# Optimization experiments

Measured on AMD Instinct MI355X. Metric: run time of the kernel, lower is better.

## Reference

```python
import jax, jax.numpy as jnp
import numpy as np

B, T, A, K, STEPS, E = 2, 16384, 128, 128, 16, 126


def soft_dirac_last(x):
    # softmax forward-replaced by one-hot(argmax), straight-through backward
    sm = jax.nn.softmax(x, axis=-1)
    hard = jax.nn.one_hot(jnp.argmax(x, axis=-1), x.shape[-1], dtype=x.dtype)
    return sm + jax.lax.stop_gradient(hard - sm)


def _encode(x, d_unit, atom_embeddings):
    # x: (B,1,T); d_unit: (A,K) unit-norm atoms
    rng = jnp.linspace(0.0, 1.0, T, dtype=x.dtype)
    kernel = d_unit[:, None, :]  # OIH
    pad = [(K // 2, K - 1 - K // 2)]  # SAME
    batch_ix = jnp.arange(B)

    def step(res, _):
        # dense feature map: correlation of residual with every atom
        fm = jax.lax.conv_general_dilated(
            res, kernel, window_strides=(1,), padding=pad,
            dimension_numbers=("NCH", "OIH", "NCH"))  # (B,A,T)
        flat = fm.reshape(B, A * T)
        fi = jnp.argmax(flat, axis=-1)                      # sparsify n_to_keep=1
        value = jnp.take_along_axis(flat, fi[:, None], axis=-1)  # (B,1)
        ai = fi // T
        ti = fi % T
        # position: soft_dirac over time of sparse fm summed over atoms
        pos_row = jnp.zeros((B, T), x.dtype).at[batch_ix, ti].set(value[:, 0])
        pd = soft_dirac_last(pos_row)
        position = jnp.sum(pd * rng[None, :], axis=-1, keepdims=True) * 20.0  # (B,1)
        # atom one-hot: soft_dirac over atom axis of sparse fm summed over time
        atom_row = jnp.zeros((B, A), x.dtype).at[batch_ix, ai].set(value[:, 0])
        ad = soft_dirac_last(atom_row)
        ae = ad @ atom_embeddings  # (B,E)
        emb = jnp.concatenate([position, value, ae], axis=-1)  # (B, 2+E)
        # matching-pursuit residual update: subtract value * atom at found shift
        recon = value * d_unit[ai]  # (B,K)
        buf = jnp.zeros((B, T + K), x.dtype)
        buf = jax.vmap(lambda bb, rr, tt: jax.lax.dynamic_update_slice(bb, rr, (tt,)))(buf, recon, ti)
        res = res - buf[:, None, K // 2:K // 2 + T]
        return res, emb

    res, embs = jax.lax.scan(step, x, None, length=STEPS)
    embs = jnp.transpose(embs, (1, 0, 2))  # (B, STEPS, 2+E)
    return embs, res


def _canonical_ordering(embs, proj):
    keys = embs @ proj  # (B, STEPS)
    order = jnp.argsort(keys, axis=-1)
    return jnp.take_along_axis(embs, order[:, :, None], axis=1)


def setup_inputs() -> dict:
    key = jax.random.key(0)
    ks = jax.random.split(key, 5)
    return {
        "a": jax.random.normal(ks[0], (B, 1, T), jnp.float32),
        "b": jax.random.normal(ks[1], (B, 1, T), jnp.float32),
        "d": jax.random.normal(ks[2], (A, K), jnp.float32),
        "atom_embeddings": jax.random.normal(ks[3], (A, E), jnp.float32) * 0.1,
        "ordering_proj": jax.random.normal(ks[4], (128,), jnp.float32),
    }


def reference(a, b, d, atom_embeddings, ordering_proj):
    d_unit = d / (jnp.linalg.norm(d, axis=-1, keepdims=True) + 1e-8)
    ae, a_res = _encode(a, d_unit, atom_embeddings)
    be, b_res = _encode(b, d_unit, atom_embeddings)
    ae = _canonical_ordering(ae, ordering_proj)
    be = _canonical_ordering(be, ordering_proj)
    a_norm = jnp.linalg.norm(a_res.reshape(-1, T), axis=-1)
    b_norm = jnp.linalg.norm(b_res.reshape(-1, T), axis=-1)
    return jnp.mean((ae - be) ** 2) + jnp.mean(jnp.abs(a_norm - b_norm))
```

## Files before the change

kernel.cpp:

```cpp
#include <hip/hip_runtime.h>
#include <math.h>

#define T_DIM 16384
#define A_DIM 128
#define K_DIM 128
#define N_STEPS 16
#define E_DIM 126
#define NSEQ 4

#define NPT0 512
#define NAT8 16
#define TT 256
#define NTT 64
#define HB 8192
#define RL_LEN 8319
#define SS_LEN 383
#define SPAD 16

#define PIDX(i) ((i) + ((i) >> 5))

#define NB_STEP0 (NPT0 * NSEQ)
#define NB_INC   (65 * NSEQ)
#define NB_TOTAL (NB_STEP0 + NB_INC + 1)

#define SM_U64 4448

__device__ inline unsigned long long pack_vi(float v, int fi) {
    unsigned int b = __float_as_uint(v);
    b = (b & 0x80000000u) ? ~b : (b | 0x80000000u);
    return ((unsigned long long)b << 32) | (unsigned int)(~fi);
}
__device__ inline void unpack_vi(unsigned long long p, float* v, int* fi) {
    unsigned int lo = (unsigned int)(p & 0xffffffffu);
    unsigned int b = (unsigned int)(p >> 32);
    unsigned int fb = (b & 0x80000000u) ? (b & 0x7fffffffu) : ~b;
    *v = __uint_as_float(fb);
    *fi = (int)(~lo);
}
__device__ inline unsigned long long u64max(unsigned long long a, unsigned long long b) {
    return a > b ? a : b;
}
__device__ inline unsigned long long pollu64(const unsigned long long* p) {
    unsigned long long v = __hip_atomic_load(p, __ATOMIC_RELAXED,
                                             __HIP_MEMORY_SCOPE_AGENT);
    while (v == 0ULL) {
        __builtin_amdgcn_s_sleep(1);
        v = __hip_atomic_load(p, __ATOMIC_RELAXED, __HIP_MEMORY_SCOPE_AGENT);
    }
    return v;
}

__global__ __launch_bounds__(256) void k_prep(
    const float* __restrict__ d, float* __restrict__ du,
    unsigned long long* __restrict__ arena) {
    int blk = blockIdx.x, tid = threadIdx.x;
    if (blk < 128) {
        __shared__ float s[128];
        float v = 0.0f;
        if (tid < 128) { v = d[blk * K_DIM + tid]; s[tid] = v * v; }
        __syncthreads();
        for (int off = 64; off > 0; off >>= 1) {
            if (tid < off) s[tid] += s[tid + off];
            __syncthreads();
        }
        if (tid < 128) du[blk * K_DIM + tid] = v / (sqrtf(s[0]) + 1e-8f);
    } else {
        int zb = blk - 128;
        for (int i = zb * 256 + tid; i < 31744; i += 64 * 256)
            arena[2048 + i] = 0ULL;
        if (blk == 128) {
            int* ctrl = (int*)(arena + 33792);
            if (tid < NSEQ) {
                ctrl[tid * 32] = 0;
                ((float*)ctrl)[160 + tid * 32] = 0.0f;
            }
            if (tid == 4) ctrl[128] = 0;
        }
    }
}

__device__ inline unsigned long long tile16(
    const float* __restrict__ duP, const float* __restrict__ rsh,
    int L0, int a_lo, int t_lo, int tid, unsigned long long* red4) {
    float acc[4][4];
    #pragma unroll
    for (int i = 0; i < 4; i++)
        #pragma unroll
        for (int j = 0; j < 4; j++) acc[i][j] = 0.0f;
    float r[8];
    #pragma unroll
    for (int m = 0; m < 8; m++) r[m] = rsh[PIDX(L0 + m)];
    #pragma unroll 4
    for (int k = 0; k < K_DIM; k += 4) {
        float dA[4][4];
        #pragma unroll
        for (int i = 0; i < 4; i++)
            *(float4*)dA[i] = *(const float4*)(duP + i * K_DIM + k);
        #pragma unroll
        for (int dk = 0; dk < 4; dk++) {
            #pragma unroll
            for (int i = 0; i < 4; i++) {
                float s = dA[i][dk];
                #pragma unroll
                for (int j = 0; j < 4; j++)
                    acc[i][j] = fmaf(s, r[j + dk], acc[i][j]);
            }
        }
        r[0] = r[4]; r[1] = r[5]; r[2] = r[6]; r[3] = r[7];
        #pragma unroll
        for (int m = 0; m < 4; m++) r[4 + m] = rsh[PIDX(L0 + k + 8 + m)];
    }
    float bv = -INFINITY;
    int bi = 0x7fffffff;
    #pragma unroll
    for (int i = 0; i < 4; i++) {
        int aa = a_lo + i;
        #pragma unroll
        for (int j = 0; j < 4; j++) {
            int fi = aa * T_DIM + t_lo + j;
            float v = acc[i][j];
            if (v > bv || (v == bv && fi < bi)) { bv = v; bi = fi; }
        }
    }
    #pragma unroll
    for (int off = 32; off > 0; off >>= 1) {
        float v2 = __shfl_down(bv, off);
        int   i2 = __shfl_down(bi, off);
        if (v2 > bv || (v2 == bv && i2 < bi)) { bv = v2; bi = i2; }
    }
    if ((tid & 63) == 0) red4[tid >> 6] = pack_vi(bv, bi);
    __syncthreads();
    if (tid == 0) {
        unsigned long long m = red4[0];
        #pragma unroll
        for (int w = 1; w < 4; w++) m = u64max(m, red4[w]);
        red4[0] = m;
    }
    __syncthreads();
    return red4[0];
}

__device__ inline unsigned long long tile8(
    const float* __restrict__ duP, const float* __restrict__ rsh,
    int L0, int a_lo, int t_lo, int tid, unsigned long long* red4) {
    float acc[2][4];
    #pragma unroll
    for (int i = 0; i < 2; i++)
        #pragma unroll
        for (int j = 0; j < 4; j++) acc[i][j] = 0.0f;
    float r[8];
    #pragma unroll
    for (int m = 0; m < 8; m++) r[m] = rsh[PIDX(L0 + m)];
    #pragma unroll 4
    for (int k = 0; k < K_DIM; k += 4) {
        float dA[2][4];
        #pragma unroll
        for (int i = 0; i < 2; i++)
            *(float4*)dA[i] = *(const float4*)(duP + i * K_DIM + k);
        #pragma unroll
        for (int dk = 0; dk < 4; dk++) {
            #pragma unroll
            for (int i = 0; i < 2; i++) {
                float s = dA[i][dk];
                #pragma unroll
                for (int j = 0; j < 4; j++)
                    acc[i][j] = fmaf(s, r[j + dk], acc[i][j]);
            }
        }
        r[0] = r[4]; r[1] = r[5]; r[2] = r[6]; r[3] = r[7];
        #pragma unroll
        for (int m = 0; m < 4; m++) r[4 + m] = rsh[PIDX(L0 + k + 8 + m)];
    }
    float bv = -INFINITY;
    int bi = 0x7fffffff;
    #pragma unroll
    for (int i = 0; i < 2; i++) {
        int aa = a_lo + i;
        #pragma unroll
        for (int j = 0; j < 4; j++) {
            int fi = aa * T_DIM + t_lo + j;
            float v = acc[i][j];
            if (v > bv || (v == bv && fi < bi)) { bv = v; bi = fi; }
        }
    }
    #pragma unroll
    for (int off = 32; off > 0; off >>= 1) {
        float v2 = __shfl_down(bv, off);
        int   i2 = __shfl_down(bi, off);
        if (v2 > bv || (v2 == bv && i2 < bi)) { bv = v2; bi = i2; }
    }
    if ((tid & 63) == 0) red4[tid >> 6] = pack_vi(bv, bi);
    __syncthreads();
    if (tid == 0) {
        unsigned long long m = red4[0];
        #pragma unroll
        for (int w = 1; w < 4; w++) m = u64max(m, red4[w]);
        red4[0] = m;
    }
    __syncthreads();
    return red4[0];
}

__global__ __launch_bounds__(256) void k_mega(
    const float* __restrict__ a, const float* __restrict__ b,
    const float* __restrict__ du, const float* __restrict__ ae,
    const float* __restrict__ proj, float* __restrict__ emb,
    unsigned long long* __restrict__ arena, float* __restrict__ out) {

    __shared__ unsigned long long SMEM[SM_U64];
    unsigned long long* pmax = arena;
    unsigned long long* dsl  = arena + 2048;
    unsigned long long* wsl  = arena + 32768;
    unsigned long long* w0   = arena + 33728;
    int*   cnt   = (int*)(arena + 33792);
    int*   done  = cnt + 128;
    float* norm2 = (float*)cnt + 160;

    int blk = blockIdx.x;
    int tid = threadIdx.x;

    if (blk < NB_STEP0) {
        int seq = blk >> 9;
        int idx = blk & 511;
        int a_base = (idx >> 6) * 16;
        int t0 = (idx & 63) * TT;
        float* rsh = (float*)SMEM;
        unsigned long long* pm_sh = SMEM + 256;
        unsigned long long* red4  = SMEM + 512;
        int* flag = (int*)(SMEM + 516);

        const float* x = (seq < 2 ? a : b) + (seq & 1) * T_DIM;
        for (int i = tid; i < SS_LEN; i += 256) {
            int t = t0 - 64 + i;
            rsh[PIDX(i)] = (t >= 0 && t < T_DIM) ? x[t] : 0.0f;
        }
        __syncthreads();
        int tg = tid & 63;
        int ag = __builtin_amdgcn_readfirstlane(tid >> 6);
        unsigned long long p = tile16(du + (a_base + ag * 4) * K_DIM, rsh,
                                      4 * tg, a_base + ag * 4, t0 + 4 * tg,
                                      tid, red4);
        if (tid == 0) {
            pmax[seq * NPT0 + idx] = p;
            __threadfence();
            flag[0] = (atomicAdd(&cnt[seq * 32], 1) == NPT0 - 1);
        }
        __syncthreads();
        if (!flag[0]) return;

        __threadfence();
        pm_sh[tid] = u64max(pmax[seq * NPT0 + tid], pmax[seq * NPT0 + 256 + tid]);
        __syncthreads();
        for (int off = 128; off > 0; off >>= 1) {
            if (tid < off) pm_sh[tid] = u64max(pm_sh[tid], pm_sh[tid + off]);
            __syncthreads();
        }
        float value; int fi;
        unpack_vi(pm_sh[0], &value, &fi);
        int ai = fi >> 14, ti = fi & (T_DIM - 1);
        int pos_idx = value > 0.0f ? ti : 0;
        int atom_idx = value > 0.0f ? ai : 0;
        float* e = emb + (seq * N_STEPS + 0) * 128;
        if (tid == 0) {
            e[0] = ((float)pos_idx / (float)(T_DIM - 1)) * 20.0f;
            e[1] = value;
        }
        if (tid >= 2 && tid < 2 + E_DIM) e[tid] = ae[atom_idx * E_DIM + tid - 2];
        __syncthreads();
        __threadfence();
        if (tid == 0) atomicExch(&w0[seq * SPAD], pm_sh[0]);
        return;
    }

    if (blk < NB_STEP0 + NB_INC) {
        int r = blk - NB_STEP0;
        int seq = r / 65;
        int sub = r - seq * 65;

        if (sub == 64) {
            unsigned long long* table   = SMEM;
            unsigned long long* poll_sh = SMEM + 512;
            unsigned long long* red4    = SMEM + 548;
            unsigned long long* wbc     = SMEM + 552;

            if (tid == 0) wbc[0] = pollu64(&w0[seq * SPAD]);
            __syncthreads();
            __threadfence();
            for (int i = tid; i < NPT0; i += 256) table[i] = pmax[seq * NPT0 + i];
            float v0; int fi0;
            unpack_vi(wbc[0], &v0, &fi0);
            int ti = fi0 & (T_DIM - 1);
            int lo = ti - 127; if (lo < 0) lo = 0;
            int hi = ti + 128; if (hi > T_DIM) hi = T_DIM;
            __syncthreads();

            for (int step = 1; step < N_STEPS; step++) {
                int T0 = lo >> 8, T1 = T0 + 1;
                bool hasT1 = (T1 < NTT) && (T1 * TT < hi);
                if (tid < 32) {
                    if (((tid & 1) == 0) || hasT1)
                        poll_sh[tid] = pollu64(
                            &dsl[(((step - 1) * NSEQ + seq) * 32 + tid) * SPAD]);
                }
                __syncthreads();
                if (tid < 16) {
                    int at16 = tid >> 1, ts = tid & 1;
                    if (ts == 0 || hasT1)
                        table[at16 * 64 + (ts ? T1 : T0)] =
                            u64max(poll_sh[at16 * 4 + ts], poll_sh[at16 * 4 + 2 + ts]);
                }
                __syncthreads();
                unsigned long long m = u64max(table[tid], table[tid + 256]);
                #pragma unroll
                for (int off = 32; off > 0; off >>= 1)
                    m = u64max(m, __shfl_down(m, off));
                if ((tid & 63) == 0) red4[tid >> 6] = m;
                __syncthreads();
                if (tid == 0) {
                    unsigned long long w = red4[0];
                    #pragma unroll
                    for (int j = 1; j < 4; j++) w = u64max(w, red4[j]);
                    red4[0] = w;
                    atomicExch(&wsl[((step - 1) * NSEQ + seq) * SPAD], w);
                }
                __syncthreads();
                float value; int fi;
                unpack_vi(red4[0], &value, &fi);
                int wt = fi & (T_DIM - 1);
                int wa = fi >> 14;
                int pos_idx = value > 0.0f ? wt : 0;
                int atom_idx = value > 0.0f ? wa : 0;
                float* e = emb + (seq * N_STEPS + step) * 128;
                if (tid == 0) {
                    e[0] = ((float)pos_idx / (float)(T_DIM - 1)) * 20.0f;
                    e[1] = value;
                }
                if (tid >= 2 && tid < 128) e[tid] = ae[atom_idx * E_DIM + tid - 2];
                lo = wt - 127; if (lo < 0) lo = 0;
                hi = wt + 128; if (hi > T_DIM) hi = T_DIM;
            }
            __syncthreads();
            __threadfence();
            if (tid == 0) atomicAdd(done, 1);
            return;
        }

        int atile = sub >> 2;
        int half = (sub >> 1) & 1;
        int par = sub & 1;
        int a_base = atile * 8;
        int base = half * HB;
        float* resL = (float*)SMEM;
        unsigned long long* red4 = SMEM + 4304;
        unsigned long long* wshp = SMEM + 4308;
        float* snorm = (float*)(SMEM + 4320);

        const float* x = (seq < 2 ? a : b) + (seq & 1) * T_DIM;
        for (int i = tid; i < RL_LEN; i += 256) {
            int t = base - 64 + i;
            resL[PIDX(i)] = (t >= 0 && t < T_DIM) ? x[t] : 0.0f;
        }
        if (tid == 0) wshp[0] = pollu64(&w0[seq * SPAD]);
        __syncthreads();
        float v0; int fi0;
        unpack_vi(wshp[0], &v0, &fi0);
        int ti0 = fi0 & (T_DIM - 1), ai0 = fi0 >> 14;
        if (tid < 128) {
            int t = ti0 - 64 + tid;
            if (t >= 0 && t < T_DIM) {
                int L = t - base + 64;
                if (L >= 0 && L < RL_LEN) {
                    float rr = resL[PIDX(L)];
                    resL[PIDX(L)] = __fsub_rn(rr, __fmul_rn(v0, du[ai0 * K_DIM + tid]));
                }
            }
        }
        __syncthreads();
        int lo = ti0 - 127; if (lo < 0) lo = 0;
        int hi = ti0 + 128; if (hi > T_DIM) hi = T_DIM;

        for (int step = 1; step < N_STEPS; step++) {
            int T0 = lo >> 8, T1 = T0 + 1;
            int cand = -1;
            if (((T0 & 1) == par) && ((T0 >> 5) == half)) cand = T0;
            else if (T1 < NTT && ((T1 & 1) == par) && ((T1 >> 5) == half) &&
                     T1 * TT < hi) cand = T1;

            if (cand >= 0) {
                int t0 = cand * TT;
                int tg = tid & 63;
                int ag = __builtin_amdgcn_readfirstlane(tid >> 6);
                unsigned long long p = tile8(
                    du + (a_base + ag * 2) * K_DIM, resL,
                    (t0 - base) + 4 * tg, a_base + ag * 2, t0 + 4 * tg, tid, red4);
                if (tid == 0)
                    atomicExch(&dsl[(((step - 1) * NSEQ + seq) * 32 +
                                     atile * 2 + (cand == T1 ? 1 : 0)) * SPAD], p);
            }
            if (tid == 0) wshp[0] = pollu64(&wsl[((step - 1) * NSEQ + seq) * SPAD]);
            __syncthreads();
            float value; int fi;
            unpack_vi(wshp[0], &value, &fi);
            int wt = fi & (T_DIM - 1);
            int wa = fi >> 14;
            if (tid < 128) {
                int t = wt - 64 + tid;
                if (t >= 0 && t < T_DIM) {
                    int L = t - base + 64;
                    if (L >= 0 && L < RL_LEN) {
                        float rr = resL[PIDX(L)];
                        resL[PIDX(L)] = __fsub_rn(rr, __fmul_rn(value, du[wa * K_DIM + tid]));
                    }
                }
            }
            __syncthreads();
            lo = wt - 127; if (lo < 0) lo = 0;
            hi = wt + 128; if (hi > T_DIM) hi = T_DIM;
        }

        if (atile == 0 && par == 0) {
            float s = 0.0f;
            for (int t = tid; t < HB; t += 256) {
                float v = resL[PIDX(t + 64)];
                s = fmaf(v, v, s);
            }
            snorm[tid] = s;
            __syncthreads();
            for (int off = 128; off > 0; off >>= 1) {
                if (tid < off) snorm[tid] += snorm[tid + off];
                __syncthreads();
            }
            if (tid == 0) {
                float old = atomicAdd(&norm2[seq * 32], snorm[0]);
                if (__float_as_uint(old) != 0xFFFFFFFFu)
                    atomicAdd(done, 1);
            }
        }
        return;
    }

    {
        float* keys  = (float*)SMEM;
        int*   order = (int*)(SMEM + 32);
        float* sh    = (float*)(SMEM + 64);
        float* norms = (float*)(SMEM + 192);

        if (tid == 0) {
            int c = __hip_atomic_load(done, __ATOMIC_RELAXED, __HIP_MEMORY_SCOPE_AGENT);
            while (c < 12) {
                __builtin_amdgcn_s_sleep(8);
                c = __hip_atomic_load(done, __ATOMIC_RELAXED, __HIP_MEMORY_SCOPE_AGENT);
            }
        }
        __syncthreads();
        __threadfence();

        if (tid < NSEQ)
            norms[tid] = sqrtf(__hip_atomic_load(&norm2[tid * 32], __ATOMIC_RELAXED,
                                                 __HIP_MEMORY_SCOPE_AGENT));
        if (tid < 64) {
            int seq = tid >> 4, st = tid & 15;
            const float* e = emb + (seq * N_STEPS + st) * 128;
            float kk = 0.0f;
            for (int dd = 0; dd < 128; dd++) kk = fmaf(e[dd], proj[dd], kk);
            keys[tid] = kk;
        }
        __syncthreads();
        if (tid < NSEQ) {
            int ord[N_STEPS];
            for (int i = 0; i < N_STEPS; i++) ord[i] = i;
            for (int i = 1; i < N_STEPS; i++) {
                int oi = ord[i];
                float kv = keys[tid * N_STEPS + oi];
                int j = i - 1;
                while (j >= 0 && keys[tid * N_STEPS + ord[j]] > kv) {
                    ord[j + 1] = ord[j]; j--;
                }
                ord[j + 1] = oi;
            }
            for (int i = 0; i < N_STEPS; i++) order[tid * N_STEPS + i] = ord[i];
        }
        __syncthreads();
        float s = 0.0f;
        #pragma unroll
        for (int t = 0; t < 16; t++) {
            int idx = tid + t * 256;
            int bq = idx >> 11;
            int st = (idx >> 7) & 15;
            int dd = idx & 127;
            float va = emb[((bq    ) * N_STEPS + order[bq * N_STEPS + st]) * 128 + dd];
            float vb = emb[((2 + bq) * N_STEPS + order[(2 + bq) * N_STEPS + st]) * 128 + dd];
            float df = va - vb;
            s = fmaf(df, df, s);
        }
        sh[tid] = s;
        __syncthreads();
        for (int off = 128; off > 0; off >>= 1) {
            if (tid < off) sh[tid] += sh[tid + off];
            __syncthreads();
        }
        if (tid == 0) {
            float mse = sh[0] / 4096.0f;
            float mad = 0.5f * (fabsf(norms[0] - norms[2]) + fabsf(norms[1] - norms[3]));
            out[0] = mse + mad;
        }
    }
}

extern "C" void kernel_launch(void* const* d_in, const int* in_sizes, int n_in,
                              void* d_out, int out_size, void* d_ws, size_t ws_size,
                              hipStream_t stream) {
    const float* a    = (const float*)d_in[0];
    const float* b    = (const float*)d_in[1];
    const float* d    = (const float*)d_in[2];
    const float* ae   = (const float*)d_in[3];
    const float* proj = (const float*)d_in[4];
    float* out = (float*)d_out;

    float* ws  = (float*)d_ws;
    float* du  = ws;
    float* emb = du + A_DIM * K_DIM;
    unsigned long long* arena = (unsigned long long*)(emb + NSEQ * N_STEPS * 128);

    k_prep<<<192, 256, 0, stream>>>(d, du, arena);
    k_mega<<<NB_TOTAL, 256, 0, stream>>>(a, b, du, ae, proj, emb, arena, out);
}
```

Measured before the change: 216.7 us.

## Replicate argmax reduction in every worker block to drop coordinator broadcast hop

Each worker block now waits on the step-0 completion counter, reads the full partial-max table itself, and at each later step polls all per-tile partial maxima and reduces them locally. The separate coordinator-to-worker winner broadcast (wsl/w0) is no longer on the critical path. This removes one global-memory round trip of cross-block latency per matching-pursuit step. In exchange every block does redundant polling and reduction and keeps a 512-entry table in shared memory, which raises shared memory use and global polling traffic.

```diff
diff --git a/kernel.cpp b/kernel.cpp
--- a/kernel.cpp
+++ b/kernel.cpp
@@ -23,7 +23,7 @@
 #define NB_INC   (65 * NSEQ)
 #define NB_TOTAL (NB_STEP0 + NB_INC + 1)
 
-#define SM_U64 4448
+#define SM_U64 4960
 
 __device__ inline unsigned long long pack_vi(float v, int fi) {
     unsigned int b = __float_as_uint(v);
@@ -48,6 +48,13 @@
         v = __hip_atomic_load(p, __ATOMIC_RELAXED, __HIP_MEMORY_SCOPE_AGENT);
     }
     return v;
+}
+__device__ inline void pollcnt(const int* p, int target) {
+    int v = __hip_atomic_load(p, __ATOMIC_RELAXED, __HIP_MEMORY_SCOPE_AGENT);
+    while (v < target) {
+        __builtin_amdgcn_s_sleep(1);
+        v = __hip_atomic_load(p, __ATOMIC_RELAXED, __HIP_MEMORY_SCOPE_AGENT);
+    }
 }
 
 __global__ __launch_bounds__(256) void k_prep(
@@ -210,7 +217,6 @@
     __shared__ unsigned long long SMEM[SM_U64];
     unsigned long long* pmax = arena;
     unsigned long long* dsl  = arena + 2048;
-    unsigned long long* wsl  = arena + 32768;
     unsigned long long* w0   = arena + 33728;
     int*   cnt   = (int*)(arena + 33792);
     int*   done  = cnt + 128;
@@ -281,18 +287,32 @@
             unsigned long long* table   = SMEM;
             unsigned long long* poll_sh = SMEM + 512;
             unsigned long long* red4    = SMEM + 548;
-            unsigned long long* wbc     = SMEM + 552;
-
-            if (tid == 0) wbc[0] = pollu64(&w0[seq * SPAD]);
+
+            if (tid == 0) pollcnt(&cnt[seq * 32], NPT0);
             __syncthreads();
             __threadfence();
             for (int i = tid; i < NPT0; i += 256) table[i] = pmax[seq * NPT0 + i];
+            __syncthreads();
+            {
+                unsigned long long m0 = u64max(table[tid], table[tid + 256]);
+                #pragma unroll
+                for (int off = 32; off > 0; off >>= 1)
+                    m0 = u64max(m0, __shfl_down(m0, off));
+                if ((tid & 63) == 0) red4[tid >> 6] = m0;
+            }
+            __syncthreads();
+            if (tid == 0) {
+                unsigned long long w = red4[0];
+                #pragma unroll
+                for (int j = 1; j < 4; j++) w = u64max(w, red4[j]);
+                red4[0] = w;
+            }
+            __syncthreads();
             float v0; int fi0;
-            unpack_vi(wbc[0], &v0, &fi0);
+            unpack_vi(red4[0], &v0, &fi0);
             int ti = fi0 & (T_DIM - 1);
             int lo = ti - 127; if (lo < 0) lo = 0;
             int hi = ti + 128; if (hi > T_DIM) hi = T_DIM;
-            __syncthreads();
 
             for (int step = 1; step < N_STEPS; step++) {
                 int T0 = lo >> 8, T1 = T0 + 1;
@@ -321,7 +341,6 @@
                     #pragma unroll
                     for (int j = 1; j < 4; j++) w = u64max(w, red4[j]);
                     red4[0] = w;
-                    atomicExch(&wsl[((step - 1) * NSEQ + seq) * SPAD], w);
                 }
                 __syncthreads();
                 float value; int fi;
@@ -351,8 +370,9 @@
         int a_base = atile * 8;
         int base = half * HB;
         float* resL = (float*)SMEM;
-        unsigned long long* red4 = SMEM + 4304;
-        unsigned long long* wshp = SMEM + 4308;
+        unsigned long long* red4   = SMEM + 4304;
+        unsigned long long* pollsh = SMEM + 4320;
+        unsigned long long* table  = SMEM + 4448;
         float* snorm = (float*)(SMEM + 4320);
 
         const float* x = (seq < 2 ? a : b) + (seq & 1) * T_DIM;
@@ -360,10 +380,28 @@
             int t = base - 64 + i;
             resL[PIDX(i)] = (t >= 0 && t < T_DIM) ? x[t] : 0.0f;
         }
-        if (tid == 0) wshp[0] = pollu64(&w0[seq * SPAD]);
+        if (tid == 0) pollcnt(&cnt[seq * 32], NPT0);
+        __syncthreads();
+        __threadfence();
+        for (int i = tid; i < NPT0; i += 256) table[i] = pmax[seq * NPT0 + i];
+        __syncthreads();
+        {
+            unsigned long long m0 = u64max(table[tid], table[tid + 256]);
+            #pragma unroll
+            for (int off = 32; off > 0; off >>= 1)
+                m0 = u64max(m0, __shfl_down(m0, off));
+            if ((tid & 63) == 0) red4[tid >> 6] = m0;
+        }
+        __syncthreads();
+        if (tid == 0) {
+            unsigned long long w = red4[0];
+            #pragma unroll
+            for (int j = 1; j < 4; j++) w = u64max(w, red4[j]);
+            red4[0] = w;
+        }
         __syncthreads();
         float v0; int fi0;
-        unpack_vi(wshp[0], &v0, &fi0);
+        unpack_vi(red4[0], &v0, &fi0);
         int ti0 = fi0 & (T_DIM - 1), ai0 = fi0 >> 14;
         if (tid < 128) {
             int t = ti0 - 64 + tid;
@@ -381,6 +419,7 @@
 
         for (int step = 1; step < N_STEPS; step++) {
             int T0 = lo >> 8, T1 = T0 + 1;
+            bool hasT1 = (T1 < NTT) && (T1 * TT < hi);
             int cand = -1;
             if (((T0 & 1) == par) && ((T0 >> 5) == half)) cand = T0;
             else if (T1 < NTT && ((T1 & 1) == par) && ((T1 >> 5) == half) &&
@@ -397,10 +436,34 @@
                     atomicExch(&dsl[(((step - 1) * NSEQ + seq) * 32 +
                                      atile * 2 + (cand == T1 ? 1 : 0)) * SPAD], p);
             }
-            if (tid == 0) wshp[0] = pollu64(&wsl[((step - 1) * NSEQ + seq) * SPAD]);
+            if (tid < 32) {
+                if (((tid & 1) == 0) || hasT1)
+                    pollsh[tid] = pollu64(
+                        &dsl[(((step - 1) * NSEQ + seq) * 32 + tid) * SPAD]);
+            }
+            __syncthreads();
+            if (tid < 16) {
+                int at16 = tid >> 1, ts = tid & 1;
+                if (ts == 0 || hasT1)
+                    table[at16 * 64 + (ts ? T1 : T0)] =
+                        u64max(pollsh[at16 * 4 + ts], pollsh[at16 * 4 + 2 + ts]);
+            }
+            __syncthreads();
+            unsigned long long m = u64max(table[tid], table[tid + 256]);
+            #pragma unroll
+            for (int off = 32; off > 0; off >>= 1)
+                m = u64max(m, __shfl_down(m, off));
+            if ((tid & 63) == 0) red4[tid >> 6] = m;
+            __syncthreads();
+            if (tid == 0) {
+                unsigned long long w = red4[0];
+                #pragma unroll
+                for (int j = 1; j < 4; j++) w = u64max(w, red4[j]);
+                red4[0] = w;
+            }
             __syncthreads();
             float value; int fi;
-            unpack_vi(wshp[0], &value, &fi);
+            unpack_vi(red4[0], &value, &fi);
             int wt = fi & (T_DIM - 1);
             int wa = fi >> 14;
             if (tid < 128) {
```

Measured after the change: 226.4 us. 4.5% more time.

## Double block size to 512 threads, stage atoms in LDS, prefetch atom loads

Applied to the files above, without the earlier changes.

Moves k_mega from 256 to 512 threads per block and halves each wave's atom count, so eight waves share a tile. The unit-norm atom rows are copied into shared memory and read from there with a one-step register prefetch, instead of coming straight from global memory. All reductions and shared-memory offsets are resized for eight waves, and the spin-wait now polls a few times before it starts sleeping. The aim is more latency hiding and less global traffic in the correlation tiles, at the cost of higher shared-memory use per block and more barrier participants.

```diff
diff --git a/kernel.cpp b/kernel.cpp
--- a/kernel.cpp
+++ b/kernel.cpp
@@ -9,13 +9,13 @@
 #define NSEQ 4
 
 #define NPT0 512
-#define NAT8 16
 #define TT 256
 #define NTT 64
 #define HB 8192
 #define RL_LEN 8319
 #define SS_LEN 383
 #define SPAD 16
+#define NTHR 512
 
 #define PIDX(i) ((i) + ((i) >> 5))
 
@@ -23,7 +23,7 @@
 #define NB_INC   (65 * NSEQ)
 #define NB_TOTAL (NB_STEP0 + NB_INC + 1)
 
-#define SM_U64 4448
+#define SM_U64 4960
 
 __device__ inline unsigned long long pack_vi(float v, int fi) {
     unsigned int b = __float_as_uint(v);
@@ -43,8 +43,9 @@
 __device__ inline unsigned long long pollu64(const unsigned long long* p) {
     unsigned long long v = __hip_atomic_load(p, __ATOMIC_RELAXED,
                                              __HIP_MEMORY_SCOPE_AGENT);
+    int spins = 0;
     while (v == 0ULL) {
-        __builtin_amdgcn_s_sleep(1);
+        if (++spins > 4) __builtin_amdgcn_s_sleep(1);
         v = __hip_atomic_load(p, __ATOMIC_RELAXED, __HIP_MEMORY_SCOPE_AGENT);
     }
     return v;
@@ -79,42 +80,55 @@
     }
 }
 
-__device__ inline unsigned long long tile16(
-    const float* __restrict__ duP, const float* __restrict__ rsh,
-    int L0, int a_lo, int t_lo, int tid, unsigned long long* red4) {
-    float acc[4][4];
+template<int APW>
+__device__ inline unsigned long long tileW(
+    const float* __restrict__ duL,
+    const float* __restrict__ rsh,
+    int L0, int a_blk, int t_lo, int tid, unsigned long long* red8) {
+    int ag = __builtin_amdgcn_readfirstlane(tid >> 6);
+    const float* dp = duL + (ag * APW) * K_DIM;
+    float acc[APW][4];
     #pragma unroll
-    for (int i = 0; i < 4; i++)
+    for (int i = 0; i < APW; i++)
         #pragma unroll
         for (int j = 0; j < 4; j++) acc[i][j] = 0.0f;
-    float r[8];
+    float r[12];
     #pragma unroll
-    for (int m = 0; m < 8; m++) r[m] = rsh[PIDX(L0 + m)];
+    for (int m = 0; m < 12; m++) r[m] = rsh[PIDX(L0 + m)];
+    float4 dnx[APW];
+    #pragma unroll
+    for (int i = 0; i < APW; i++)
+        dnx[i] = *(const float4*)(dp + i * K_DIM);
     #pragma unroll 4
     for (int k = 0; k < K_DIM; k += 4) {
-        float dA[4][4];
-        #pragma unroll
-        for (int i = 0; i < 4; i++)
-            *(float4*)dA[i] = *(const float4*)(duP + i * K_DIM + k);
+        float dc[APW][4];
+        #pragma unroll
+        for (int i = 0; i < APW; i++) *(float4*)dc[i] = dnx[i];
+        if (k + 4 < K_DIM) {
+            #pragma unroll
+            for (int i = 0; i < APW; i++)
+                dnx[i] = *(const float4*)(dp + i * K_DIM + k + 4);
+        }
         #pragma unroll
         for (int dk = 0; dk < 4; dk++) {
             #pragma unroll
-            for (int i = 0; i < 4; i++) {
-                float s = dA[i][dk];
+            for (int i = 0; i < APW; i++) {
+                float s = dc[i][dk];
                 #pragma unroll
                 for (int j = 0; j < 4; j++)
                     acc[i][j] = fmaf(s, r[j + dk], acc[i][j]);
             }
         }
-        r[0] = r[4]; r[1] = r[5]; r[2] = r[6]; r[3] = r[7];
-        #pragma unroll
-        for (int m = 0; m < 4; m++) r[4 + m] = rsh[PIDX(L0 + k + 8 + m)];
+        #pragma unroll
+        for (int m = 0; m < 8; m++) r[m] = r[4 + m];
+        #pragma unroll
+        for (int m = 0; m < 4; m++) r[8 + m] = rsh[PIDX(L0 + k + 12 + m)];
     }
     float bv = -INFINITY;
     int bi = 0x7fffffff;
     #pragma unroll
-    for (int i = 0; i < 4; i++) {
-        int aa = a_lo + i;
+    for (int i = 0; i < APW; i++) {
+        int aa = a_blk + ag * APW + i;
         #pragma unroll
         for (int j = 0; j < 4; j++) {
             int fi = aa * T_DIM + t_lo + j;
@@ -128,80 +142,19 @@
         int   i2 = __shfl_down(bi, off);
         if (v2 > bv || (v2 == bv && i2 < bi)) { bv = v2; bi = i2; }
     }
-    if ((tid & 63) == 0) red4[tid >> 6] = pack_vi(bv, bi);
+    if ((tid & 63) == 0) red8[tid >> 6] = pack_vi(bv, bi);
     __syncthreads();
     if (tid == 0) {
-        unsigned long long m = red4[0];
-        #pragma unroll
-        for (int w = 1; w < 4; w++) m = u64max(m, red4[w]);
-        red4[0] = m;
+        unsigned long long m = red8[0];
+        #pragma unroll
+        for (int w = 1; w < 8; w++) m = u64max(m, red8[w]);
+        red8[0] = m;
     }
     __syncthreads();
-    return red4[0];
-}
-
-__device__ inline unsigned long long tile8(
-    const float* __restrict__ duP, const float* __restrict__ rsh,
-    int L0, int a_lo, int t_lo, int tid, unsigned long long* red4) {
-    float acc[2][4];
-    #pragma unroll
-    for (int i = 0; i < 2; i++)
-        #pragma unroll
-        for (int j = 0; j < 4; j++) acc[i][j] = 0.0f;
-    float r[8];
-    #pragma unroll
-    for (int m = 0; m < 8; m++) r[m] = rsh[PIDX(L0 + m)];
-    #pragma unroll 4
-    for (int k = 0; k < K_DIM; k += 4) {
-        float dA[2][4];
-        #pragma unroll
-        for (int i = 0; i < 2; i++)
-            *(float4*)dA[i] = *(const float4*)(duP + i * K_DIM + k);
-        #pragma unroll
-        for (int dk = 0; dk < 4; dk++) {
-            #pragma unroll
-            for (int i = 0; i < 2; i++) {
-                float s = dA[i][dk];
-                #pragma unroll
-                for (int j = 0; j < 4; j++)
-                    acc[i][j] = fmaf(s, r[j + dk], acc[i][j]);
-            }
-        }
-        r[0] = r[4]; r[1] = r[5]; r[2] = r[6]; r[3] = r[7];
-        #pragma unroll
-        for (int m = 0; m < 4; m++) r[4 + m] = rsh[PIDX(L0 + k + 8 + m)];
-    }
-    float bv = -INFINITY;
-    int bi = 0x7fffffff;
-    #pragma unroll
-    for (int i = 0; i < 2; i++) {
-        int aa = a_lo + i;
-        #pragma unroll
-        for (int j = 0; j < 4; j++) {
-            int fi = aa * T_DIM + t_lo + j;
-            float v = acc[i][j];
-            if (v > bv || (v == bv && fi < bi)) { bv = v; bi = fi; }
-        }
-    }
-    #pragma unroll
-    for (int off = 32; off > 0; off >>= 1) {
-        float v2 = __shfl_down(bv, off);
-        int   i2 = __shfl_down(bi, off);
-        if (v2 > bv || (v2 == bv && i2 < bi)) { bv = v2; bi = i2; }
-    }
-    if ((tid & 63) == 0) red4[tid >> 6] = pack_vi(bv, bi);
-    __syncthreads();
-    if (tid == 0) {
-        unsigned long long m = red4[0];
-        #pragma unroll
-        for (int w = 1; w < 4; w++) m = u64max(m, red4[w]);
-        red4[0] = m;
-    }
-    __syncthreads();
-    return red4[0];
-}
-
-__global__ __launch_bounds__(256) void k_mega(
+    return red8[0];
+}
+
+__global__ __launch_bounds__(512, 8) void k_mega(
     const float* __restrict__ a, const float* __restrict__ b,
     const float* __restrict__ du, const float* __restrict__ ae,
     const float* __restrict__ proj, float* __restrict__ emb,
@@ -225,21 +178,22 @@
         int a_base = (idx >> 6) * 16;
         int t0 = (idx & 63) * TT;
         float* rsh = (float*)SMEM;
-        unsigned long long* pm_sh = SMEM + 256;
-        unsigned long long* red4  = SMEM + 512;
-        int* flag = (int*)(SMEM + 516);
+        unsigned long long* red8 = SMEM + 224;
+        int* flag = (int*)(SMEM + 240);
+        float* duLf = (float*)(SMEM + 256);
+        unsigned long long* pm_sh = SMEM + 1280;
 
         const float* x = (seq < 2 ? a : b) + (seq & 1) * T_DIM;
-        for (int i = tid; i < SS_LEN; i += 256) {
+        for (int i = tid; i < SS_LEN; i += NTHR) {
             int t = t0 - 64 + i;
             rsh[PIDX(i)] = (t >= 0 && t < T_DIM) ? x[t] : 0.0f;
         }
+        for (int i = tid; i < 16 * K_DIM; i += NTHR)
+            duLf[i] = du[a_base * K_DIM + i];
         __syncthreads();
         int tg = tid & 63;
-        int ag = __builtin_amdgcn_readfirstlane(tid >> 6);
-        unsigned long long p = tile16(du + (a_base + ag * 4) * K_DIM, rsh,
-                                      4 * tg, a_base + ag * 4, t0 + 4 * tg,
-                                      tid, red4);
+        unsigned long long p = tileW<2>(duLf, rsh, 4 * tg, a_base,
+                                        t0 + 4 * tg, tid, red8);
         if (tid == 0) {
             pmax[seq * NPT0 + idx] = p;
             __threadfence();
@@ -249,9 +203,9 @@
         if (!flag[0]) return;
 
         __threadfence();
-        pm_sh[tid] = u64max(pmax[seq * NPT0 + tid], pmax[seq * NPT0 + 256 + tid]);
-        __syncthreads();
-        for (int off = 128; off > 0; off >>= 1) {
+        pm_sh[tid] = pmax[seq * NPT0 + tid];
+        __syncthreads();
+        for (int off = 256; off > 0; off >>= 1) {
             if (tid < off) pm_sh[tid] = u64max(pm_sh[tid], pm_sh[tid + off]);
             __syncthreads();
         }
@@ -280,13 +234,13 @@
         if (sub == 64) {
             unsigned long long* table   = SMEM;
             unsigned long long* poll_sh = SMEM + 512;
-            unsigned long long* red4    = SMEM + 548;
-            unsigned long long* wbc     = SMEM + 552;
+            unsigned long long* red8    = SMEM + 548;
+            unsigned long long* wbc     = SMEM + 560;
 
             if (tid == 0) wbc[0] = pollu64(&w0[seq * SPAD]);
             __syncthreads();
             __threadfence();
-            for (int i = tid; i < NPT0; i += 256) table[i] = pmax[seq * NPT0 + i];
+            for (int i = tid; i < NPT0; i += NTHR) table[i] = pmax[seq * NPT0 + i];
             float v0; int fi0;
             unpack_vi(wbc[0], &v0, &fi0);
             int ti = fi0 & (T_DIM - 1);
@@ -310,22 +264,22 @@
                             u64max(poll_sh[at16 * 4 + ts], poll_sh[at16 * 4 + 2 + ts]);
                 }
                 __syncthreads();
-                unsigned long long m = u64max(table[tid], table[tid + 256]);
+                unsigned long long m = table[tid];
                 #pragma unroll
                 for (int off = 32; off > 0; off >>= 1)
                     m = u64max(m, __shfl_down(m, off));
-                if ((tid & 63) == 0) red4[tid >> 6] = m;
+                if ((tid & 63) == 0) red8[tid >> 6] = m;
                 __syncthreads();
                 if (tid == 0) {
-                    unsigned long long w = red4[0];
+                    unsigned long long w = red8[0];
                     #pragma unroll
-                    for (int j = 1; j < 4; j++) w = u64max(w, red4[j]);
-                    red4[0] = w;
+                    for (int j = 1; j < 8; j++) w = u64max(w, red8[j]);
+                    red8[0] = w;
                     atomicExch(&wsl[((step - 1) * NSEQ + seq) * SPAD], w);
                 }
                 __syncthreads();
                 float value; int fi;
-                unpack_vi(red4[0], &value, &fi);
+                unpack_vi(red8[0], &value, &fi);
                 int wt = fi & (T_DIM - 1);
                 int wa = fi >> 14;
                 int pos_idx = value > 0.0f ? wt : 0;
@@ -351,15 +305,18 @@
         int a_base = atile * 8;
         int base = half * HB;
         float* resL = (float*)SMEM;
-        unsigned long long* red4 = SMEM + 4304;
-        unsigned long long* wshp = SMEM + 4308;
+        unsigned long long* red8 = SMEM + 4304;
+        unsigned long long* wshp = SMEM + 4314;
+        float* duLf = (float*)(SMEM + 4320);
         float* snorm = (float*)(SMEM + 4320);
 
         const float* x = (seq < 2 ? a : b) + (seq & 1) * T_DIM;
-        for (int i = tid; i < RL_LEN; i += 256) {
+        for (int i = tid; i < RL_LEN; i += NTHR) {
             int t = base - 64 + i;
             resL[PIDX(i)] = (t >= 0 && t < T_DIM) ? x[t] : 0.0f;
         }
+        for (int i = tid; i < 8 * K_DIM; i += NTHR)
+            duLf[i] = du[a_base * K_DIM + i];
         if (tid == 0) wshp[0] = pollu64(&w0[seq * SPAD]);
         __syncthreads();
         float v0; int fi0;
@@ -389,10 +346,9 @@
             if (cand >= 0) {
                 int t0 = cand * TT;
                 int tg = tid & 63;
-                int ag = __builtin_amdgcn_readfirstlane(tid >> 6);
-                unsigned long long p = tile8(
-                    du + (a_base + ag * 2) * K_DIM, resL,
-                    (t0 - base) + 4 * tg, a_base + ag * 2, t0 + 4 * tg, tid, red4);
+                unsigned long long p = tileW<1>(
+                    duLf, resL, (t0 - base) + 4 * tg, a_base, t0 + 4 * tg,
+                    tid, red8);
                 if (tid == 0)
                     atomicExch(&dsl[(((step - 1) * NSEQ + seq) * 32 +
                                      atile * 2 + (cand == T1 ? 1 : 0)) * SPAD], p);
@@ -420,13 +376,13 @@
 
         if (atile == 0 && par == 0) {
             float s = 0.0f;
-            for (int t = tid; t < HB; t += 256) {
+            for (int t = tid; t < HB; t += NTHR) {
                 float v = resL[PIDX(t + 64)];
                 s = fmaf(v, v, s);
             }
             snorm[tid] = s;
             __syncthreads();
-            for (int off = 128; off > 0; off >>= 1) {
+            for (int off = 256; off > 0; off >>= 1) {
                 if (tid < off) snorm[tid] += snorm[tid + off];
                 __syncthreads();
             }
@@ -443,7 +399,7 @@
         float* keys  = (float*)SMEM;
         int*   order = (int*)(SMEM + 32);
         float* sh    = (float*)(SMEM + 64);
-        float* norms = (float*)(SMEM + 192);
+        float* norms = (float*)(SMEM + 320);
 
         if (tid == 0) {
             int c = __hip_atomic_load(done, __ATOMIC_RELAXED, __HIP_MEMORY_SCOPE_AGENT);
@@ -483,8 +439,8 @@
         __syncthreads();
         float s = 0.0f;
         #pragma unroll
-        for (int t = 0; t < 16; t++) {
-            int idx = tid + t * 256;
+        for (int t = 0; t < 8; t++) {
+            int idx = tid + t * NTHR;
             int bq = idx >> 11;
             int st = (idx >> 7) & 15;
             int dd = idx & 127;
@@ -495,7 +451,7 @@
         }
         sh[tid] = s;
         __syncthreads();
-        for (int off = 128; off > 0; off >>= 1) {
+        for (int off = 256; off > 0; off >>= 1) {
             if (tid < off) sh[tid] += sh[tid + off];
             __syncthreads();
         }
@@ -523,5 +479,5 @@
     unsigned long long* arena = (unsigned long long*)(emb + NSEQ * N_STEPS * 128);
 
     k_prep<<<192, 256, 0, stream>>>(d, du, arena);
-    k_mega<<<NB_TOTAL, 256, 0, stream>>>(a, b, du, ae, proj, emb, arena, out);
-}
+    k_mega<<<NB_TOTAL, 512, 0, stream>>>(a, b, du, ae, proj, emb, arena, out);
+}
```

Result: slower. 471.4 us (+117.5%).

## Decentralize per-step argmax reduction into worker blocks and cache atoms in LDS

Applied to the files above, without the earlier changes.

Each worker block now keeps its own copy of the per-tile max table in registers. It polls the 32 per-tile partial slots directly and reduces the global argmax itself, so it no longer waits for a coordinator block to publish a winner. This removes one global-memory round-trip of latency from every matching-pursuit step. The change also loads the block's 8 atoms into shared memory, drops the padded residual indexing in favour of float4 residual reads through a rotating register window, and spins a few times before sleeping in the poll loop. The costs are redundant reductions in every block, more shared memory, and possible LDS bank conflicts now that padding is gone.

```diff
diff --git a/kernel.cpp b/kernel.cpp
--- a/kernel.cpp
+++ b/kernel.cpp
@@ -9,11 +9,11 @@
 #define NSEQ 4
 
 #define NPT0 512
-#define NAT8 16
 #define TT 256
 #define NTT 64
 #define HB 8192
 #define RL_LEN 8319
+#define RL_ALLOC 8320
 #define SS_LEN 383
 #define SPAD 16
 
@@ -23,7 +23,7 @@
 #define NB_INC   (65 * NSEQ)
 #define NB_TOTAL (NB_STEP0 + NB_INC + 1)
 
-#define SM_U64 4448
+#define SM_U64 4720
 
 __device__ inline unsigned long long pack_vi(float v, int fi) {
     unsigned int b = __float_as_uint(v);
@@ -43,8 +43,9 @@
 __device__ inline unsigned long long pollu64(const unsigned long long* p) {
     unsigned long long v = __hip_atomic_load(p, __ATOMIC_RELAXED,
                                              __HIP_MEMORY_SCOPE_AGENT);
+    int spins = 0;
     while (v == 0ULL) {
-        __builtin_amdgcn_s_sleep(1);
+        if (++spins > 4) __builtin_amdgcn_s_sleep(1);
         v = __hip_atomic_load(p, __ATOMIC_RELAXED, __HIP_MEMORY_SCOPE_AGENT);
     }
     return v;
@@ -140,23 +141,31 @@
     return red4[0];
 }
 
-__device__ inline unsigned long long tile8(
-    const float* __restrict__ duP, const float* __restrict__ rsh,
+__device__ inline unsigned long long tile8i(
+    const float* __restrict__ duL,
+    const float* __restrict__ rsh,
     int L0, int a_lo, int t_lo, int tid, unsigned long long* red4) {
+    int ag = __builtin_amdgcn_readfirstlane(tid >> 6);
+    const float* dp = duL + (ag * 2) * K_DIM;
     float acc[2][4];
     #pragma unroll
     for (int i = 0; i < 2; i++)
         #pragma unroll
         for (int j = 0; j < 4; j++) acc[i][j] = 0.0f;
-    float r[8];
-    #pragma unroll
-    for (int m = 0; m < 8; m++) r[m] = rsh[PIDX(L0 + m)];
-    #pragma unroll 4
-    for (int k = 0; k < K_DIM; k += 4) {
-        float dA[2][4];
-        #pragma unroll
-        for (int i = 0; i < 2; i++)
-            *(float4*)dA[i] = *(const float4*)(duP + i * K_DIM + k);
+    float4 rw[3];
+    rw[0] = *(const float4*)(rsh + L0);
+    rw[1] = *(const float4*)(rsh + L0 + 4);
+    rw[2] = *(const float4*)(rsh + L0 + 8);
+    #pragma unroll
+    for (int n = 0; n < 32; n++) {
+        const int k = 4 * n;
+        float4 d0 = *(const float4*)(dp + k);
+        float4 d1 = *(const float4*)(dp + K_DIM + k);
+        const float4 ra = rw[n % 3];
+        const float4 rb = rw[(n + 1) % 3];
+        const float r[8] = {ra.x, ra.y, ra.z, ra.w, rb.x, rb.y, rb.z, rb.w};
+        const float dA[2][4] = {{d0.x, d0.y, d0.z, d0.w},
+                                {d1.x, d1.y, d1.z, d1.w}};
         #pragma unroll
         for (int dk = 0; dk < 4; dk++) {
             #pragma unroll
@@ -167,15 +176,13 @@
                     acc[i][j] = fmaf(s, r[j + dk], acc[i][j]);
             }
         }
-        r[0] = r[4]; r[1] = r[5]; r[2] = r[6]; r[3] = r[7];
-        #pragma unroll
-        for (int m = 0; m < 4; m++) r[4 + m] = rsh[PIDX(L0 + k + 8 + m)];
+        if (n < 30) rw[n % 3] = *(const float4*)(rsh + L0 + k + 12);
     }
     float bv = -INFINITY;
     int bi = 0x7fffffff;
     #pragma unroll
     for (int i = 0; i < 2; i++) {
-        int aa = a_lo + i;
+        int aa = a_lo + ag * 2 + i;
         #pragma unroll
         for (int j = 0; j < 4; j++) {
             int fi = aa * T_DIM + t_lo + j;
@@ -210,7 +217,6 @@
     __shared__ unsigned long long SMEM[SM_U64];
     unsigned long long* pmax = arena;
     unsigned long long* dsl  = arena + 2048;
-    unsigned long long* wsl  = arena + 32768;
     unsigned long long* w0   = arena + 33728;
     int*   cnt   = (int*)(arena + 33792);
     int*   done  = cnt + 128;
@@ -281,7 +287,7 @@
             unsigned long long* table   = SMEM;
             unsigned long long* poll_sh = SMEM + 512;
             unsigned long long* red4    = SMEM + 548;
-            unsigned long long* wbc     = SMEM + 552;
+            unsigned long long* wbc     = SMEM + 556;
 
             if (tid == 0) wbc[0] = pollu64(&w0[seq * SPAD]);
             __syncthreads();
@@ -321,7 +327,6 @@
                     #pragma unroll
                     for (int j = 1; j < 4; j++) w = u64max(w, red4[j]);
                     red4[0] = w;
-                    atomicExch(&wsl[((step - 1) * NSEQ + seq) * SPAD], w);
                 }
                 __syncthreads();
                 float value; int fi;
@@ -351,17 +356,26 @@
         int a_base = atile * 8;
         int base = half * HB;
         float* resL = (float*)SMEM;
-        unsigned long long* red4 = SMEM + 4304;
-        unsigned long long* wshp = SMEM + 4308;
-        float* snorm = (float*)(SMEM + 4320);
+        unsigned long long* red4   = SMEM + 4160;
+        unsigned long long* pollsh = SMEM + 4168;
+        unsigned long long* wshp   = SMEM + 4200;
+        float* duLf  = (float*)(SMEM + 4208);
+        float* snorm = (float*)(SMEM + 4208);
 
         const float* x = (seq < 2 ? a : b) + (seq & 1) * T_DIM;
-        for (int i = tid; i < RL_LEN; i += 256) {
+        for (int i = tid; i < RL_ALLOC; i += 256) {
             int t = base - 64 + i;
-            resL[PIDX(i)] = (t >= 0 && t < T_DIM) ? x[t] : 0.0f;
+            resL[i] = (t >= 0 && t < T_DIM) ? x[t] : 0.0f;
+        }
+        if (tid < 256) {
+            ((float4*)duLf)[tid] = ((const float4*)(du + a_base * K_DIM))[tid];
         }
         if (tid == 0) wshp[0] = pollu64(&w0[seq * SPAD]);
         __syncthreads();
+        __threadfence();
+        unsigned long long tA = pmax[seq * NPT0 + tid];
+        unsigned long long tB = pmax[seq * NPT0 + 256 + tid];
+
         float v0; int fi0;
         unpack_vi(wshp[0], &v0, &fi0);
         int ti0 = fi0 & (T_DIM - 1), ai0 = fi0 >> 14;
@@ -370,8 +384,8 @@
             if (t >= 0 && t < T_DIM) {
                 int L = t - base + 64;
                 if (L >= 0 && L < RL_LEN) {
-                    float rr = resL[PIDX(L)];
-                    resL[PIDX(L)] = __fsub_rn(rr, __fmul_rn(v0, du[ai0 * K_DIM + tid]));
+                    float rr = resL[L];
+                    resL[L] = __fsub_rn(rr, __fmul_rn(v0, du[ai0 * K_DIM + tid]));
                 }
             }
         }
@@ -381,26 +395,54 @@
 
         for (int step = 1; step < N_STEPS; step++) {
             int T0 = lo >> 8, T1 = T0 + 1;
+            bool hasT1 = (T1 < NTT) && (T1 * TT < hi);
             int cand = -1;
             if (((T0 & 1) == par) && ((T0 >> 5) == half)) cand = T0;
-            else if (T1 < NTT && ((T1 & 1) == par) && ((T1 >> 5) == half) &&
-                     T1 * TT < hi) cand = T1;
+            else if (hasT1 && ((T1 & 1) == par) && ((T1 >> 5) == half)) cand = T1;
 
             if (cand >= 0) {
                 int t0 = cand * TT;
                 int tg = tid & 63;
-                int ag = __builtin_amdgcn_readfirstlane(tid >> 6);
-                unsigned long long p = tile8(
-                    du + (a_base + ag * 2) * K_DIM, resL,
-                    (t0 - base) + 4 * tg, a_base + ag * 2, t0 + 4 * tg, tid, red4);
+                unsigned long long p = tile8i(
+                    duLf, resL, (t0 - base) + 4 * tg, a_base, t0 + 4 * tg,
+                    tid, red4);
                 if (tid == 0)
                     atomicExch(&dsl[(((step - 1) * NSEQ + seq) * 32 +
                                      atile * 2 + (cand == T1 ? 1 : 0)) * SPAD], p);
             }
-            if (tid == 0) wshp[0] = pollu64(&wsl[((step - 1) * NSEQ + seq) * SPAD]);
+            if (tid < 32) {
+                if (((tid & 1) == 0) || hasT1)
+                    pollsh[tid] = pollu64(
+                        &dsl[(((step - 1) * NSEQ + seq) * 32 + tid) * SPAD]);
+            }
+            __syncthreads();
+            {
+                int tt = tid & 63;
+                int at16A = tid >> 6;
+                int at16B = at16A + 4;
+                if (tt == T0) {
+                    tA = u64max(pollsh[at16A * 4 + 0], pollsh[at16A * 4 + 2]);
+                    tB = u64max(pollsh[at16B * 4 + 0], pollsh[at16B * 4 + 2]);
+                } else if (hasT1 && tt == T1) {
+                    tA = u64max(pollsh[at16A * 4 + 1], pollsh[at16A * 4 + 3]);
+                    tB = u64max(pollsh[at16B * 4 + 1], pollsh[at16B * 4 + 3]);
+                }
+            }
+            unsigned long long m = u64max(tA, tB);
+            #pragma unroll
+            for (int off = 32; off > 0; off >>= 1)
+                m = u64max(m, __shfl_down(m, off));
+            if ((tid & 63) == 0) red4[tid >> 6] = m;
+            __syncthreads();
+            if (tid == 0) {
+                unsigned long long w = red4[0];
+                #pragma unroll
+                for (int j = 1; j < 4; j++) w = u64max(w, red4[j]);
+                red4[0] = w;
+            }
             __syncthreads();
             float value; int fi;
-            unpack_vi(wshp[0], &value, &fi);
+            unpack_vi(red4[0], &value, &fi);
             int wt = fi & (T_DIM - 1);
             int wa = fi >> 14;
             if (tid < 128) {
@@ -408,8 +450,8 @@
                 if (t >= 0 && t < T_DIM) {
                     int L = t - base + 64;
                     if (L >= 0 && L < RL_LEN) {
-                        float rr = resL[PIDX(L)];
-                        resL[PIDX(L)] = __fsub_rn(rr, __fmul_rn(value, du[wa * K_DIM + tid]));
+                        float rr = resL[L];
+                        resL[L] = __fsub_rn(rr, __fmul_rn(value, du[wa * K_DIM + tid]));
                     }
                 }
             }
@@ -421,7 +463,7 @@
         if (atile == 0 && par == 0) {
             float s = 0.0f;
             for (int t = tid; t < HB; t += 256) {
-                float v = resL[PIDX(t + 64)];
+                float v = resL[t + 64];
                 s = fmaf(v, v, s);
             }
             snorm[tid] = s;
```

New measurement: 364.1 us. 68.0% more time.
